# Kernel optimization log

Hardware: AMD Instinct MI355X
Metric: run time of the kernel (lower is better)

The kernel has to match this reference:

```python
import jax, jax.numpy as jnp
import numpy as np

B, C, INNER, H, W = 32, 256, 128, 32, 32
EPS = 1e-5


def _conv1x1(x, w):
    # x: (B, Cin, H, W); w: (Cout, Cin) -> (B, Cout, H, W)
    return jnp.einsum('bchw,oc->bohw', x, w)


def _attend(q, k, v):
    # q,k: (B, D, H, W); v: (B, C, H, W)
    b, d, h, w = q.shape
    n = h * w
    qf = q.reshape(b, d, n).transpose(0, 2, 1)            # (B, N, D)
    kf = k.reshape(b, d, n).transpose(0, 2, 1)            # (B, N, D)
    vf = v.reshape(b, v.shape[1], n).transpose(0, 2, 1)   # (B, N, C)
    scale = 1.0 / jnp.sqrt(jnp.asarray(d, qf.dtype))
    attn = jax.nn.softmax(jnp.einsum('bnd,bmd->bnm', qf, kf) * scale, axis=-1)
    of = jnp.einsum('bnm,bmc->bnc', attn, vf)             # (B, N, C)
    return of.transpose(0, 2, 1).reshape(b, -1, h, w)


def _layernorm(x, w, b):
    # Normalize over (C, H, W) jointly; affine params broadcast from (C,1,1).
    mu = jnp.mean(x, axis=(1, 2, 3), keepdims=True)
    var = jnp.mean(jnp.square(x - mu), axis=(1, 2, 3), keepdims=True)
    return (x - mu) * jax.lax.rsqrt(var + EPS) * w[None] + b[None]


def setup_inputs() -> dict:
    key = jax.random.key(0)
    ks = jax.random.split(key, 10)
    s = 0.02
    return {
        'fs': jax.random.normal(ks[0], (B, C, H, W), jnp.float32),
        'fi': jax.random.normal(ks[1], (B, C, H, W), jnp.float32),
        'qs_w': jax.random.normal(ks[2], (INNER, C), jnp.float32) * s,
        'ks_w': jax.random.normal(ks[3], (INNER, C), jnp.float32) * s,
        'vs_w': jax.random.normal(ks[4], (C, C), jnp.float32) * s,
        'qi_w': jax.random.normal(ks[5], (INNER, C), jnp.float32) * s,
        'ki_w': jax.random.normal(ks[6], (INNER, C), jnp.float32) * s,
        'vi_w': jax.random.normal(ks[7], (C, C), jnp.float32) * s,
        'fuse_w': jax.random.normal(ks[8], (C, 2 * C), jnp.float32) * s,
        'fuse_b': jnp.zeros((C,), jnp.float32),
        'ln_s_w': jnp.ones((C, 1, 1), jnp.float32),
        'ln_s_b': jnp.zeros((C, 1, 1), jnp.float32),
        'ln_i_w': jnp.ones((C, 1, 1), jnp.float32),
        'ln_i_b': jnp.zeros((C, 1, 1), jnp.float32),
    }


def reference(fs, fi, qs_w, ks_w, vs_w, qi_w, ki_w, vi_w,
              fuse_w, fuse_b, ln_s_w, ln_s_b, ln_i_w, ln_i_b):
    # sketch queries attend over image keys/values
    s2i = _attend(_conv1x1(fs, qs_w), _conv1x1(fi, ki_w), _conv1x1(fi, vi_w))
    # image queries attend over sketch keys/values
    i2s = _attend(_conv1x1(fi, qi_w), _conv1x1(fs, ks_w), _conv1x1(fs, vs_w))

    def fuse(x):
        return jax.nn.relu(_conv1x1(x, fuse_w) + fuse_b[None, :, None, None])

    fs_out = _layernorm(fuse(jnp.concatenate([fs, i2s], axis=1)) + fs, ln_s_w, ln_s_b)
    fi_out = _layernorm(fuse(jnp.concatenate([fi, s2i], axis=1)) + fi, ln_i_w, ln_i_b)
    return (fs_out, fi_out)
```

## Files before the change

### kernel.cpp

```cpp
#include <hip/hip_runtime.h>

typedef unsigned short u16;
typedef unsigned int   u32;

#define B_   32
#define C_   256
#define N_   1024
#define CN_  (C_*N_)
#define EPS_ 1e-5f

typedef __attribute__((ext_vector_type(8))) short  short8;
typedef __attribute__((ext_vector_type(4))) float  f32x4;

__device__ __forceinline__ float b2f(u16 u){
  union { u32 u; float f; } c; c.u = ((u32)u) << 16; return c.f;
}
__device__ __forceinline__ u16 f2b(float f){
  union { float f; u32 u; } c; c.f = f;
  u32 u = c.u;
  return (u16)((u + 0x7FFFu + ((u >> 16) & 1u)) >> 16);
}

struct F4v { float v[4]; };

__device__ __forceinline__ F4v ld4g(const void* p, long i, int bf){
  F4v r;
  if (bf){
    ushort4 u = *(const ushort4*)((const u16*)p + i);
    r.v[0]=b2f(u.x); r.v[1]=b2f(u.y); r.v[2]=b2f(u.z); r.v[3]=b2f(u.w);
  } else {
    float4 f = *(const float4*)((const float*)p + i);
    r.v[0]=f.x; r.v[1]=f.y; r.v[2]=f.z; r.v[3]=f.w;
  }
  return r;
}
__device__ __forceinline__ float ld1g(const void* p, long i, int bf){
  return bf ? b2f(((const u16*)p)[i]) : ((const float*)p)[i];
}
__device__ __forceinline__ void st1g(void* p, long i, float v, int bf){
  if (bf) ((u16*)p)[i] = f2b(v); else ((float*)p)[i] = v;
}
__device__ __forceinline__ void st4g(void* p, long i, const float* v, int bf){
  if (bf){
    ushort4 u;
    u.x=f2b(v[0]); u.y=f2b(v[1]); u.z=f2b(v[2]); u.w=f2b(v[3]);
    *(ushort4*)((u16*)p + i) = u;
  } else {
    *(float4*)((float*)p + i) = make_float4(v[0],v[1],v[2],v[3]);
  }
}
__device__ __forceinline__ int sniff_bf(const void* lnw){
  return (*(const u32*)lnw == 0x3F803F80u) ? 1 : 0;
}

__global__ __launch_bounds__(256) void k_prep_w(
    const void* qs, const void* ks, const void* vs,
    const void* qi, const void* ki, const void* vi,
    const void* fw, const void* lnw,
    u16* __restrict__ Wcat, u16* __restrict__ fuseWb, float* __restrict__ stats)
{
  const int bf = sniff_bf(lnw);
  if (blockIdx.x == 0 && threadIdx.x < 128) stats[threadIdx.x] = 0.0f;
  const long idx = ((long)blockIdx.x*256 + threadIdx.x) * 4;
  if (idx < 262144){
    const int side = (int)(idx >> 17);
    const int rem  = (int)(idx & 131071);
    const int row  = rem >> 8, col = rem & 255;
    const void* src; int r2;
    if (row < 128)      { src = side ? qi : qs; r2 = row; }
    else if (row < 256) { src = side ? ki : ks; r2 = row - 128; }
    else                { src = side ? vi : vs; r2 = row - 256; }
    F4v v = ld4g(src, (long)r2*256 + col, bf);
    ushort4 u; u.x=f2b(v.v[0]); u.y=f2b(v.v[1]); u.z=f2b(v.v[2]); u.w=f2b(v.v[3]);
    *(ushort4*)&Wcat[idx] = u;
  } else {
    const long j = idx - 262144;
    F4v v = ld4g(fw, j, bf);
    ushort4 u; u.x=f2b(v.v[0]); u.y=f2b(v.v[1]); u.z=f2b(v.v[2]); u.w=f2b(v.v[3]);
    *(ushort4*)&fuseWb[j] = u;
  }
}

__global__ __launch_bounds__(256) void k_prep_t(
    const void* fs, const void* fi, const void* lnw, u16* __restrict__ Ft)
{
  const int bf = sniff_bf(lnw);
  const int nt = blockIdx.x, ct = blockIdx.y, bs = blockIdx.z;
  const int b = bs >> 1, side = bs & 1;
  const void* F = side ? fi : fs;
  const int t = threadIdx.x;
  __shared__ u16 T[64][72];
  const int c0 = ct << 6, n0 = nt << 6;
  const int nc = (t & 15) << 2, cl = t >> 4;
  #pragma unroll
  for (int p = 0; p < 4; p++){
    const int c = cl + (p << 4);
    F4v v = ld4g(F, ((long)b*C_ + c0 + c)*N_ + n0 + nc, bf);
    T[nc  ][c] = f2b(v.v[0]);
    T[nc+1][c] = f2b(v.v[1]);
    T[nc+2][c] = f2b(v.v[2]);
    T[nc+3][c] = f2b(v.v[3]);
  }
  __syncthreads();
  const int nl = t >> 2, cc = (t & 3) << 4;
  float4 x0 = *(const float4*)&T[nl][cc];
  float4 x1 = *(const float4*)&T[nl][cc + 8];
  u16* dst = Ft + ((long)bs << 18) + (long)(n0 + nl)*256 + c0 + cc;
  *(float4*)dst = x0;
  *(float4*)(dst + 8) = x1;
}

__global__ __launch_bounds__(256) void k_proj(
    const u16* __restrict__ Wcat, const u16* __restrict__ Ft,
    u16* __restrict__ QKp, u16* __restrict__ Vp)
{
  const int nt = blockIdx.x;
  const int ot = blockIdx.y;
  const int bs = blockIdx.z;
  const int side = bs & 1;
  const int t = threadIdx.x;
  const int wv = t >> 6, li = t & 15, qd = (t >> 4) & 3;
  const int o0 = (ot << 7) + (wv << 5);
  const int n0 = nt << 7;

  __shared__ __align__(16) u16 VT[128][136];

  const u16* ap = Wcat + ((long)side*512 + o0 + li)*256 + qd*8;
  const u16* bp = Ft + ((long)bs << 18) + (long)(n0 + li)*256 + qd*8;

  const f32x4 z4 = {0.f,0.f,0.f,0.f};
  f32x4 acc[2][8];
  #pragma unroll
  for (int i = 0; i < 2; i++)
    #pragma unroll
    for (int j = 0; j < 8; j++) acc[i][j] = z4;

  for (int ks = 0; ks < 8; ks++){
    const int ko = ks*32;
    short8 a0 = *(const short8*)(ap + ko);
    short8 a1 = *(const short8*)(ap + 16*256 + ko);
    short8 bfr[8];
    #pragma unroll
    for (int j = 0; j < 8; j++) bfr[j] = *(const short8*)(bp + (long)j*16*256 + ko);
    #pragma unroll
    for (int j = 0; j < 8; j++){
      acc[0][j] = __builtin_amdgcn_mfma_f32_16x16x32_bf16(a0, bfr[j], acc[0][j], 0, 0, 0);
      acc[1][j] = __builtin_amdgcn_mfma_f32_16x16x32_bf16(a1, bfr[j], acc[1][j], 0, 0, 0);
    }
  }

  if (o0 < 256){
    u16* base = QKp + ((long)bs << 18);
    #pragma unroll
    for (int mi = 0; mi < 2; mi++){
      const int ocol = o0 + mi*16 + qd*4;
      #pragma unroll
      for (int j = 0; j < 8; j++){
        const int n = n0 + j*16 + li;
        ushort4 u;
        u.x = f2b(acc[mi][j][0]); u.y = f2b(acc[mi][j][1]);
        u.z = f2b(acc[mi][j][2]); u.w = f2b(acc[mi][j][3]);
        *(ushort4*)&base[(long)n*256 + ocol] = u;
      }
    }
  } else {
    #pragma unroll
    for (int mi = 0; mi < 2; mi++){
      #pragma unroll
      for (int j = 0; j < 8; j++){
        const int n = j*16 + li;
        #pragma unroll
        for (int r = 0; r < 4; r++){
          const int cl = (wv<<5) + mi*16 + qd*4 + r;
          VT[cl][n] = f2b(acc[mi][j][r]);
        }
      }
    }
    __syncthreads();
    const int c0g = (ot - 2) << 7;
    u16* baseV = Vp + ((long)bs << 18);
    const int rb   = t >> 4;
    const int c16  = t & 15;
    #pragma unroll
    for (int ch = 0; ch < 8; ch++){
      const int r = rb + (ch << 4);
      float4 x = *(const float4*)&VT[r][c16*8];
      *(float4*)&baseV[(long)(c0g + r)*N_ + n0 + c16*8] = x;
    }
  }
}

#define ATTN_STEP(MT, KCUR, KNXT)                                              \
{                                                                              \
  const int m0s = (MT) << 6;                                                   \
                       \
  short8 va[8];                                                                \
  {                                                                            \
    const u16* vrow = Vb + (long)(cb + li)*N_ + m0s + qd*8;                    \
    _Pragma("unroll")                                                          \
    for (int i4 = 0; i4 < 4; i4++){                                            \
      va[i4*2  ] = *(const short8*)(vrow + (long)i4*16*N_);                    \
      va[i4*2+1] = *(const short8*)(vrow + (long)i4*16*N_ + 32);               \
    }                                                                          \
  }                                                                            \
                  \
  {                                                                            \
    const int m0n = (((MT)+1) & 15) << 6;                                      \
    const u16* krow = Kb + (long)(m0n + (wv<<4) + li)*256 + qd*8;              \
    _Pragma("unroll")                                                          \
    for (int kk = 0; kk < 4; kk++)                                             \
      KNXT[kk] = *(const short8*)(krow + kk*32);                               \
  }                                                                            \
                                \
  f32x4 sf[4];                                                                 \
  sf[0]=z4; sf[1]=z4; sf[2]=z4; sf[3]=z4;                                      \
  __builtin_amdgcn_s_setprio(1);                                               \
  _Pragma("unroll")                                                            \
  for (int j4 = 0; j4 < 4; j4++)                                               \
    _Pragma("unroll")                                                          \
    for (int kk = 0; kk < 4; kk++)                                             \
      sf[j4] = __builtin_amdgcn_mfma_f32_16x16x32_bf16(qf[j4][kk], KCUR[kk], sf[j4], 0, 0, 0); \
  __builtin_amdgcn_s_setprio(0);                                               \
                \
  u16 (*Pb)[72] = Pt[(MT) & 1];                                                \
  _Pragma("unroll")                                                            \
  for (int j4 = 0; j4 < 4; j4++){                                              \
    float p0 = exp2f(fminf(sf[j4][0]*scale2, 86.0f));                          \
    float p1 = exp2f(fminf(sf[j4][1]*scale2, 86.0f));                          \
    float p2 = exp2f(fminf(sf[j4][2]*scale2, 86.0f));                          \
    float p3 = exp2f(fminf(sf[j4][3]*scale2, 86.0f));                          \
    rs[j4][0] += p0; rs[j4][1] += p1;                                          \
    rs[j4][2] += p2; rs[j4][3] += p3;                                          \
    u32 pk0, pk1;                                                              \
    asm("v_cvt_pk_bf16_f32 %0, %1, %2" : "=v"(pk0) : "v"(p0), "v"(p1));        \
    asm("v_cvt_pk_bf16_f32 %0, %1, %2" : "=v"(pk1) : "v"(p2), "v"(p3));        \
    const int rb  = (j4<<4) + (qd<<2);                                         \
    const int col = (wv<<4) + li;                                              \
    Pb[rb  ][col] = (u16)(pk0 & 0xFFFFu);                                      \
    Pb[rb+1][col] = (u16)(pk0 >> 16);                                          \
    Pb[rb+2][col] = (u16)(pk1 & 0xFFFFu);                                      \
    Pb[rb+3][col] = (u16)(pk1 >> 16);                                          \
  }                                                                            \
      \
  asm volatile("s_waitcnt lgkmcnt(0)\n\ts_barrier" ::: "memory");              \
                                            \
  __builtin_amdgcn_s_setprio(1);                                               \
  _Pragma("unroll")                                                            \
  for (int j4 = 0; j4 < 4; j4++){                                              \
    short8 pb0 = *(const short8*)&Pb[(j4<<4) + li][qd*8];                      \
    short8 pb1 = *(const short8*)&Pb[(j4<<4) + li][qd*8 + 32];                 \
    _Pragma("unroll")                                                          \
    for (int i4 = 0; i4 < 4; i4++){                                            \
      accO[i4][j4] = __builtin_amdgcn_mfma_f32_16x16x32_bf16(va[i4*2  ], pb0, accO[i4][j4], 0, 0, 0); \
      accO[i4][j4] = __builtin_amdgcn_mfma_f32_16x16x32_bf16(va[i4*2+1], pb1, accO[i4][j4], 0, 0, 0); \
    }                                                                          \
  }                                                                            \
  __builtin_amdgcn_s_setprio(0);                                               \
}

__global__ __launch_bounds__(256) void k_attn(
    const u16* __restrict__ QKp, const u16* __restrict__ Vp, u16* __restrict__ AOt)
{
  const int id   = blockIdx.x;
  const int loc  = id >> 3;
  const int pair = ((id & 7) << 3) | (loc >> 4);
  const int nt   = loc & 15;
  const int b  = pair >> 1, tt = pair & 1;
  const int qside = 1 - tt, kvside = tt;
  const u16* Qb = QKp + (((long)(b*2+qside)) << 18);
  const u16* Kb = QKp + (((long)(b*2+kvside)) << 18) + 128;
  const u16* Vb = Vp  + (((long)(b*2+kvside)) << 18);

  const int t  = threadIdx.x;
  const int wv = t >> 6;
  const int li = t & 15;
  const int qd = (t >> 4) & 3;
  const int n0 = nt << 6;
  const int cb = wv << 6;

  __shared__ __align__(16) u16 Pt[2][64][72];
  __shared__ float lSp[4][64];

  short8 qf[4][4];
  #pragma unroll
  for (int j4 = 0; j4 < 4; j4++){
    const u16* qrow = Qb + (long)(n0 + (j4<<4) + li)*256 + qd*8;
    #pragma unroll
    for (int kk = 0; kk < 4; kk++) qf[j4][kk] = *(const short8*)(qrow + kk*32);
  }

  const f32x4 z4 = {0.f, 0.f, 0.f, 0.f};
  f32x4 accO[4][4];
  #pragma unroll
  for (int i = 0; i < 4; i++)
    #pragma unroll
    for (int j = 0; j < 4; j++) accO[i][j] = z4;
  float rs[4][4];
  #pragma unroll
  for (int i = 0; i < 4; i++)
    #pragma unroll
    for (int r = 0; r < 4; r++) rs[i][r] = 0.0f;
  const float scale2 = 0.12751742f;

  short8 kfA[4], kfB[4];
  {
    const u16* krow = Kb + (long)((wv<<4) + li)*256 + qd*8;
    #pragma unroll
    for (int kk = 0; kk < 4; kk++) kfA[kk] = *(const short8*)(krow + kk*32);
  }

  for (int mt2 = 0; mt2 < 16; mt2 += 2){
    ATTN_STEP(mt2,     kfA, kfB)
    ATTN_STEP(mt2 + 1, kfB, kfA)
  }

  #pragma unroll
  for (int j4 = 0; j4 < 4; j4++){
    #pragma unroll
    for (int r = 0; r < 4; r++){
      float s = rs[j4][r];
      s += __shfl_xor(s, 1, 64);
      s += __shfl_xor(s, 2, 64);
      s += __shfl_xor(s, 4, 64);
      s += __shfl_xor(s, 8, 64);
      if (li == 0) lSp[wv][(j4<<4) + (qd<<2) + r] = s;
    }
  }
  __syncthreads();
  float linv[4];
  #pragma unroll
  for (int j4 = 0; j4 < 4; j4++){
    const int q = (j4<<4) + li;
    linv[j4] = 1.0f / (lSp[0][q] + lSp[1][q] + lSp[2][q] + lSp[3][q]);
  }
  u16* aob = AOt + (((long)(b*2+tt)) << 18);
  #pragma unroll
  for (int i4 = 0; i4 < 4; i4++){
    #pragma unroll
    for (int j4 = 0; j4 < 4; j4++){
      const int n = n0 + (j4<<4) + li;
      ushort4 u;
      u.x = f2b(accO[i4][j4][0] * linv[j4]);
      u.y = f2b(accO[i4][j4][1] * linv[j4]);
      u.z = f2b(accO[i4][j4][2] * linv[j4]);
      u.w = f2b(accO[i4][j4][3] * linv[j4]);
      *(ushort4*)&aob[(long)n*256 + cb + (i4<<4) + (qd<<2)] = u;
    }
  }
}

__global__ __launch_bounds__(256) void k_fuse(
    const void* fs, const void* fi, const u16* __restrict__ fuseWb,
    const void* fbias, const u16* __restrict__ Ft, const u16* __restrict__ AOt,
    void* out, float* __restrict__ stats, const void* lnw)
{
  const int bf = sniff_bf(lnw);
  const int nt = blockIdx.x;
  const int ot = blockIdx.y;
  const int bw = blockIdx.z;
  const int b = bw >> 1, w = bw & 1;
  const void* F = w ? fi : fs;
  const int t = threadIdx.x;
  const int wv = t >> 6, li = t & 15, qd = (t >> 4) & 3;
  const int o0 = ot << 7;
  const int nb = (nt << 7) + (wv << 5);

  const u16* xp1 = Ft  + ((long)bw << 18) + (long)(nb + li)*256 + qd*8;
  const u16* xp2 = AOt + ((long)bw << 18) + (long)(nb + li)*256 + qd*8;
  const u16* wp = fuseWb + (long)(o0 + li)*512 + qd*8;

  const f32x4 z4 = {0.f,0.f,0.f,0.f};
  f32x4 acc[2][8];
  #pragma unroll
  for (int i = 0; i < 2; i++)
    #pragma unroll
    for (int j = 0; j < 8; j++) acc[i][j] = z4;

  for (int ks = 0; ks < 16; ks++){
    const u16* xp = (ks < 8) ? (xp1 + ks*32) : (xp2 + (ks-8)*32);
    const int ko = ks*32;
    short8 xa0 = *(const short8*)(xp);
    short8 xa1 = *(const short8*)(xp + 16*256);
    short8 wfr[8];
    #pragma unroll
    for (int j = 0; j < 8; j++) wfr[j] = *(const short8*)(wp + (long)j*16*512 + ko);
    #pragma unroll
    for (int j = 0; j < 8; j++){
      acc[0][j] = __builtin_amdgcn_mfma_f32_16x16x32_bf16(xa0, wfr[j], acc[0][j], 0, 0, 0);
      acc[1][j] = __builtin_amdgcn_mfma_f32_16x16x32_bf16(xa1, wfr[j], acc[1][j], 0, 0, 0);
    }
  }

  __shared__ float rbuf[8];
  float s1 = 0.0f, s2 = 0.0f;
  #pragma unroll
  for (int j = 0; j < 8; j++){
    const int o = o0 + j*16 + li;
    const float bias = ld1g(fbias, o, bf);
    #pragma unroll
    for (int mi = 0; mi < 2; mi++){
      const int n = nb + mi*16 + (qd<<2);
      F4v rv = ld4g(F, ((long)b*C_ + o)*N_ + n, bf);
      float y[4];
      #pragma unroll
      for (int r = 0; r < 4; r++){
        float v = acc[mi][j][r] + bias;
        v = v > 0.0f ? v : 0.0f;
        v += rv.v[r];
        y[r] = v;
        s1 += v; s2 += v*v;
      }
      st4g(out, ((long)w*B_ + b)*CN_ + (long)o*N_ + n, y, bf);
    }
  }
  #pragma unroll
  for (int off = 32; off > 0; off >>= 1){
    s1 += __shfl_down(s1, off, 64);
    s2 += __shfl_down(s2, off, 64);
  }
  const int lane = t & 63;
  if (lane == 0){ rbuf[wv*2] = s1; rbuf[wv*2+1] = s2; }
  __syncthreads();
  if (t == 0){
    atomicAdd(&stats[bw*2  ], rbuf[0]+rbuf[2]+rbuf[4]+rbuf[6]);
    atomicAdd(&stats[bw*2+1], rbuf[1]+rbuf[3]+rbuf[5]+rbuf[7]);
  }
}

__global__ __launch_bounds__(256) void k_ln(
    void* out, const float* __restrict__ stats,
    const void* lsw, const void* lsb, const void* liw, const void* lib)
{
  const int bf = sniff_bf(lsw);
  const long g = ((long)blockIdx.x*256 + threadIdx.x) * 4;
  const long half = (long)B_*CN_;
  const int w = (g >= half) ? 1 : 0;
  const long rem = g - (long)w*half;
  const int b  = (int)(rem >> 18);
  const int cn = (int)(rem & (CN_-1));
  const int c  = cn >> 10;
  const float s1v = stats[(b*2+w)*2], s2v = stats[(b*2+w)*2+1];
  const float inv = 1.0f / (float)CN_;
  const float mean = s1v * inv;
  const float var  = s2v * inv - mean*mean;
  const float rstd = rsqrtf(var + EPS_);
  const float lw = ld1g(w ? liw : lsw, c, bf);
  const float lb = ld1g(w ? lib : lsb, c, bf);
  F4v x = ld4g(out, g, bf);
  float vv[4];
  #pragma unroll
  for (int j = 0; j < 4; j++) vv[j] = (x.v[j] - mean)*rstd*lw + lb;
  st4g(out, g, vv, bf);
}

extern "C" void kernel_launch(void* const* d_in, const int* in_sizes, int n_in,
                              void* d_out, int out_size, void* d_ws, size_t ws_size,
                              hipStream_t stream)
{
  const void* fs     = d_in[0];
  const void* fi     = d_in[1];
  const void* qs_w   = d_in[2];
  const void* ks_w   = d_in[3];
  const void* vs_w   = d_in[4];
  const void* qi_w   = d_in[5];
  const void* ki_w   = d_in[6];
  const void* vi_w   = d_in[7];
  const void* fuse_w = d_in[8];
  const void* fuse_b = d_in[9];
  const void* ln_s_w = d_in[10];
  const void* ln_s_b = d_in[11];
  const void* ln_i_w = d_in[12];
  const void* ln_i_b = d_in[13];

  char* ws = (char*)d_ws;
  float* stats  = (float*)ws;
  u16*   Wcat   = (u16*)(ws + 4096);
  u16*   fuseWb = (u16*)(ws + 4096 + 524288);
  u16*   Ft     = (u16*)(ws + (1u<<20));
  u16*   QKp    = (u16*)(ws + (1u<<20) + (1u<<25));
  u16*   Vp     = (u16*)(ws + (1u<<20) + 2u*(1u<<25));
  u16*   AOt    = (u16*)(ws + (1u<<20) + 3u*(1u<<25));

  k_prep_w<<<dim3(384), dim3(256), 0, stream>>>(
      qs_w, ks_w, vs_w, qi_w, ki_w, vi_w, fuse_w, ln_s_w, Wcat, fuseWb, stats);
  k_prep_t<<<dim3(16,4,64), dim3(256), 0, stream>>>(fs, fi, ln_s_w, Ft);
  k_proj<<<dim3(8,4,64), dim3(256), 0, stream>>>(Wcat, Ft, QKp, Vp);
  k_attn<<<dim3(1024), dim3(256), 0, stream>>>(QKp, Vp, AOt);
  k_fuse<<<dim3(8,2,64), dim3(256), 0, stream>>>(
      fs, fi, fuseWb, fuse_b, Ft, AOt, d_out, stats, ln_s_w);
  k_ln<<<dim3(16384), dim3(256), 0, stream>>>(
      d_out, stats, ln_s_w, ln_s_b, ln_i_w, ln_i_b);
}
```

Baseline: 456.2 us.

## Fold softmax scale into Q weights, halve attention query tile, retile fuse GEMM

The softmax scale (log2e/sqrt(d)) is folded into the bf16 Q projection weights, so the attention inner loop no longer multiplies every score. The attention kernel now processes 32 queries per block instead of 64, doubling the grid to 2048 blocks and cutting register use per thread, at the cost of re-streaming K and V twice as often. The fuse GEMM is retiled so each block covers 64 positions by all 256 outputs (4x4 MFMA tiles per wave) instead of 128 positions by 128 outputs. Rounding the pre-scaled weights to bf16 slightly changes numerics.

```diff
diff --git a/kernel.cpp b/kernel.cpp
--- a/kernel.cpp
+++ b/kernel.cpp
@@ -8,6 +8,7 @@
 #define N_   1024
 #define CN_  (C_*N_)
 #define EPS_ 1e-5f
+#define SCALE2 0.12751742f
 
 typedef __attribute__((ext_vector_type(8))) short  short8;
 typedef __attribute__((ext_vector_type(4))) float  f32x4;
@@ -66,12 +67,13 @@
     const int side = (int)(idx >> 17);
     const int rem  = (int)(idx & 131071);
     const int row  = rem >> 8, col = rem & 255;
-    const void* src; int r2;
-    if (row < 128)      { src = side ? qi : qs; r2 = row; }
+    const void* src; int r2; float sc = 1.0f;
+    if (row < 128)      { src = side ? qi : qs; r2 = row; sc = SCALE2; }
     else if (row < 256) { src = side ? ki : ks; r2 = row - 128; }
     else                { src = side ? vi : vs; r2 = row - 256; }
     F4v v = ld4g(src, (long)r2*256 + col, bf);
-    ushort4 u; u.x=f2b(v.v[0]); u.y=f2b(v.v[1]); u.z=f2b(v.v[2]); u.w=f2b(v.v[3]);
+    ushort4 u;
+    u.x=f2b(v.v[0]*sc); u.y=f2b(v.v[1]*sc); u.z=f2b(v.v[2]*sc); u.w=f2b(v.v[3]*sc);
     *(ushort4*)&Wcat[idx] = u;
   } else {
     const long j = idx - 262144;
@@ -211,24 +213,24 @@
     for (int kk = 0; kk < 4; kk++)                                             \
       KNXT[kk] = *(const short8*)(krow + kk*32);                               \
   }                                                                            \
-                                \
-  f32x4 sf[4];                                                                 \
-  sf[0]=z4; sf[1]=z4; sf[2]=z4; sf[3]=z4;                                      \
+                                    \
+  f32x4 sf[2];                                                                 \
+  sf[0]=z4; sf[1]=z4;                                                          \
   __builtin_amdgcn_s_setprio(1);                                               \
   _Pragma("unroll")                                                            \
-  for (int j4 = 0; j4 < 4; j4++)                                               \
+  for (int j4 = 0; j4 < 2; j4++)                                               \
     _Pragma("unroll")                                                          \
     for (int kk = 0; kk < 4; kk++)                                             \
       sf[j4] = __builtin_amdgcn_mfma_f32_16x16x32_bf16(qf[j4][kk], KCUR[kk], sf[j4], 0, 0, 0); \
   __builtin_amdgcn_s_setprio(0);                                               \
-                \
+    \
   u16 (*Pb)[72] = Pt[(MT) & 1];                                                \
   _Pragma("unroll")                                                            \
-  for (int j4 = 0; j4 < 4; j4++){                                              \
-    float p0 = exp2f(fminf(sf[j4][0]*scale2, 86.0f));                          \
-    float p1 = exp2f(fminf(sf[j4][1]*scale2, 86.0f));                          \
-    float p2 = exp2f(fminf(sf[j4][2]*scale2, 86.0f));                          \
-    float p3 = exp2f(fminf(sf[j4][3]*scale2, 86.0f));                          \
+  for (int j4 = 0; j4 < 2; j4++){                                              \
+    float p0 = exp2f(fminf(sf[j4][0], 86.0f));                                 \
+    float p1 = exp2f(fminf(sf[j4][1], 86.0f));                                 \
+    float p2 = exp2f(fminf(sf[j4][2], 86.0f));                                 \
+    float p3 = exp2f(fminf(sf[j4][3], 86.0f));                                 \
     rs[j4][0] += p0; rs[j4][1] += p1;                                          \
     rs[j4][2] += p2; rs[j4][3] += p3;                                          \
     u32 pk0, pk1;                                                              \
@@ -243,10 +245,10 @@
   }                                                                            \
       \
   asm volatile("s_waitcnt lgkmcnt(0)\n\ts_barrier" ::: "memory");              \
-                                            \
+                                  \
   __builtin_amdgcn_s_setprio(1);                                               \
   _Pragma("unroll")                                                            \
-  for (int j4 = 0; j4 < 4; j4++){                                              \
+  for (int j4 = 0; j4 < 2; j4++){                                              \
     short8 pb0 = *(const short8*)&Pb[(j4<<4) + li][qd*8];                      \
     short8 pb1 = *(const short8*)&Pb[(j4<<4) + li][qd*8 + 32];                 \
     _Pragma("unroll")                                                          \
@@ -263,8 +265,8 @@
 {
   const int id   = blockIdx.x;
   const int loc  = id >> 3;
-  const int pair = ((id & 7) << 3) | (loc >> 4);
-  const int nt   = loc & 15;
+  const int pair = ((id & 7) << 3) | (loc >> 5);
+  const int nt   = loc & 31;
   const int b  = pair >> 1, tt = pair & 1;
   const int qside = 1 - tt, kvside = tt;
   const u16* Qb = QKp + (((long)(b*2+qside)) << 18);
@@ -275,32 +277,31 @@
   const int wv = t >> 6;
   const int li = t & 15;
   const int qd = (t >> 4) & 3;
-  const int n0 = nt << 6;
+  const int n0 = nt << 5;
   const int cb = wv << 6;
 
-  __shared__ __align__(16) u16 Pt[2][64][72];
-  __shared__ float lSp[4][64];
-
-  short8 qf[4][4];
-  #pragma unroll
-  for (int j4 = 0; j4 < 4; j4++){
+  __shared__ __align__(16) u16 Pt[2][32][72];
+  __shared__ float lSp[4][32];
+
+  short8 qf[2][4];
+  #pragma unroll
+  for (int j4 = 0; j4 < 2; j4++){
     const u16* qrow = Qb + (long)(n0 + (j4<<4) + li)*256 + qd*8;
     #pragma unroll
     for (int kk = 0; kk < 4; kk++) qf[j4][kk] = *(const short8*)(qrow + kk*32);
   }
 
   const f32x4 z4 = {0.f, 0.f, 0.f, 0.f};
-  f32x4 accO[4][4];
+  f32x4 accO[4][2];
   #pragma unroll
   for (int i = 0; i < 4; i++)
     #pragma unroll
-    for (int j = 0; j < 4; j++) accO[i][j] = z4;
-  float rs[4][4];
-  #pragma unroll
-  for (int i = 0; i < 4; i++)
+    for (int j = 0; j < 2; j++) accO[i][j] = z4;
+  float rs[2][4];
+  #pragma unroll
+  for (int i = 0; i < 2; i++)
     #pragma unroll
     for (int r = 0; r < 4; r++) rs[i][r] = 0.0f;
-  const float scale2 = 0.12751742f;
 
   short8 kfA[4], kfB[4];
   {
@@ -315,7 +316,7 @@
   }
 
   #pragma unroll
-  for (int j4 = 0; j4 < 4; j4++){
+  for (int j4 = 0; j4 < 2; j4++){
     #pragma unroll
     for (int r = 0; r < 4; r++){
       float s = rs[j4][r];
@@ -327,9 +328,9 @@
     }
   }
   __syncthreads();
-  float linv[4];
-  #pragma unroll
-  for (int j4 = 0; j4 < 4; j4++){
+  float linv[2];
+  #pragma unroll
+  for (int j4 = 0; j4 < 2; j4++){
     const int q = (j4<<4) + li;
     linv[j4] = 1.0f / (lSp[0][q] + lSp[1][q] + lSp[2][q] + lSp[3][q]);
   }
@@ -337,7 +338,7 @@
   #pragma unroll
   for (int i4 = 0; i4 < 4; i4++){
     #pragma unroll
-    for (int j4 = 0; j4 < 4; j4++){
+    for (int j4 = 0; j4 < 2; j4++){
       const int n = n0 + (j4<<4) + li;
       ushort4 u;
       u.x = f2b(accO[i4][j4][0] * linv[j4]);
@@ -356,49 +357,49 @@
 {
   const int bf = sniff_bf(lnw);
   const int nt = blockIdx.x;
-  const int ot = blockIdx.y;
-  const int bw = blockIdx.z;
+  const int bw = blockIdx.y;
   const int b = bw >> 1, w = bw & 1;
   const void* F = w ? fi : fs;
   const int t = threadIdx.x;
   const int wv = t >> 6, li = t & 15, qd = (t >> 4) & 3;
-  const int o0 = ot << 7;
-  const int nb = (nt << 7) + (wv << 5);
+  const int nb = nt << 6;
+  const int ow = wv << 6;
 
   const u16* xp1 = Ft  + ((long)bw << 18) + (long)(nb + li)*256 + qd*8;
   const u16* xp2 = AOt + ((long)bw << 18) + (long)(nb + li)*256 + qd*8;
-  const u16* wp = fuseWb + (long)(o0 + li)*512 + qd*8;
+  const u16* wp = fuseWb + (long)(ow + li)*512 + qd*8;
 
   const f32x4 z4 = {0.f,0.f,0.f,0.f};
-  f32x4 acc[2][8];
-  #pragma unroll
-  for (int i = 0; i < 2; i++)
-    #pragma unroll
-    for (int j = 0; j < 8; j++) acc[i][j] = z4;
+  f32x4 acc[4][4];
+  #pragma unroll
+  for (int i = 0; i < 4; i++)
+    #pragma unroll
+    for (int j = 0; j < 4; j++) acc[i][j] = z4;
 
   for (int ks = 0; ks < 16; ks++){
     const u16* xp = (ks < 8) ? (xp1 + ks*32) : (xp2 + (ks-8)*32);
     const int ko = ks*32;
-    short8 xa0 = *(const short8*)(xp);
-    short8 xa1 = *(const short8*)(xp + 16*256);
-    short8 wfr[8];
-    #pragma unroll
-    for (int j = 0; j < 8; j++) wfr[j] = *(const short8*)(wp + (long)j*16*512 + ko);
-    #pragma unroll
-    for (int j = 0; j < 8; j++){
-      acc[0][j] = __builtin_amdgcn_mfma_f32_16x16x32_bf16(xa0, wfr[j], acc[0][j], 0, 0, 0);
-      acc[1][j] = __builtin_amdgcn_mfma_f32_16x16x32_bf16(xa1, wfr[j], acc[1][j], 0, 0, 0);
-    }
+    short8 xa[4];
+    #pragma unroll
+    for (int mi = 0; mi < 4; mi++) xa[mi] = *(const short8*)(xp + (long)mi*16*256);
+    short8 wf[4];
+    #pragma unroll
+    for (int j = 0; j < 4; j++) wf[j] = *(const short8*)(wp + (long)j*16*512 + ko);
+    #pragma unroll
+    for (int mi = 0; mi < 4; mi++)
+      #pragma unroll
+      for (int j = 0; j < 4; j++)
+        acc[mi][j] = __builtin_amdgcn_mfma_f32_16x16x32_bf16(xa[mi], wf[j], acc[mi][j], 0, 0, 0);
   }
 
   __shared__ float rbuf[8];
   float s1 = 0.0f, s2 = 0.0f;
   #pragma unroll
-  for (int j = 0; j < 8; j++){
-    const int o = o0 + j*16 + li;
+  for (int j = 0; j < 4; j++){
+    const int o = ow + j*16 + li;
     const float bias = ld1g(fbias, o, bf);
     #pragma unroll
-    for (int mi = 0; mi < 2; mi++){
+    for (int mi = 0; mi < 4; mi++){
       const int n = nb + mi*16 + (qd<<2);
       F4v rv = ld4g(F, ((long)b*C_ + o)*N_ + n, bf);
       float y[4];
@@ -485,8 +486,8 @@
       qs_w, ks_w, vs_w, qi_w, ki_w, vi_w, fuse_w, ln_s_w, Wcat, fuseWb, stats);
   k_prep_t<<<dim3(16,4,64), dim3(256), 0, stream>>>(fs, fi, ln_s_w, Ft);
   k_proj<<<dim3(8,4,64), dim3(256), 0, stream>>>(Wcat, Ft, QKp, Vp);
-  k_attn<<<dim3(1024), dim3(256), 0, stream>>>(QKp, Vp, AOt);
-  k_fuse<<<dim3(8,2,64), dim3(256), 0, stream>>>(
+  k_attn<<<dim3(2048), dim3(256), 0, stream>>>(QKp, Vp, AOt);
+  k_fuse<<<dim3(16,64), dim3(256), 0, stream>>>(
       fs, fi, fuseWb, fuse_b, Ft, AOt, d_out, stats, ln_s_w);
   k_ln<<<dim3(16384), dim3(256), 0, stream>>>(
       d_out, stats, ln_s_w, ln_s_b, ln_i_w, ln_i_b);
```

After: 514.1 us. 1.13x slower.
